# Kernel optimization log

Measured on AMD Instinct MI355X. Metric: run time of the kernel, lower is better.

The kernel has to match this reference:

```python
import jax, jax.numpy as jnp
from jax import lax
import numpy as np

I, H, B, S = 512, 1024, 64, 512


def setup_inputs() -> dict:
    key = jax.random.key(0)
    ks = jax.random.split(key, 10)
    xav = lambda k, shape: jax.random.uniform(k, shape, jnp.float32, -1.0, 1.0) * jnp.sqrt(6.0 / (shape[0] + shape[1]))
    return {
        "x": jax.random.normal(ks[0], (B, S, I), jnp.float32),
        "wii": xav(ks[1], (I, H)), "bii": jnp.zeros((H,), jnp.float32),
        "whi": xav(ks[2], (H, H)), "bhi": jnp.zeros((H,), jnp.float32),
        "wif": xav(ks[3], (I, H)), "bif": jnp.zeros((H,), jnp.float32),
        "whf": xav(ks[4], (H, H)), "bhf": jnp.zeros((H,), jnp.float32),
        "wig": xav(ks[5], (I, H)), "big": jnp.zeros((H,), jnp.float32),
        "whg": xav(ks[6], (H, H)), "bhg": jnp.zeros((H,), jnp.float32),
        "wio": xav(ks[7], (I, H)), "bio": jnp.zeros((H,), jnp.float32),
        "who": xav(ks[8], (H, H)), "bho": jnp.zeros((H,), jnp.float32),
    }


def reference(x, wii, bii, whi, bhi, wif, bif, whf, bhf,
              wig, big, whg, bhg, wio, bio, who, bho):
    b, s, _ = x.shape
    h = wii.shape[1]
    # Fuse the four per-gate GEMMs into single (I,4H) / (H,4H) GEMMs — same math.
    Wx = jnp.concatenate([wii, wif, wig, wio], axis=1)   # (I, 4H)
    Wh = jnp.concatenate([whi, whf, whg, who], axis=1)   # (H, 4H)
    bb = jnp.concatenate([bii + bhi, bif + bhf, big + bhg, bio + bho])  # (4H,)
    xs = jnp.swapaxes(x, 0, 1)                            # (S, B, I)
    x_proj = jnp.einsum('sbi,ik->sbk', xs, Wx) + bb       # (S, B, 4H)

    def step(carry, xp):
        h_t, c_t = carry
        gates = xp + h_t @ Wh                             # (B, 4H)
        i_t, f_t, g_t, o_t = jnp.split(gates, 4, axis=-1)
        i_t = jax.nn.sigmoid(i_t)
        f_t = jax.nn.sigmoid(f_t)
        g_t = jnp.tanh(g_t)
        o_t = jax.nn.sigmoid(o_t)
        c_t = f_t * c_t + i_t * g_t
        h_t = o_t * jnp.tanh(c_t)
        return (h_t, c_t), None

    h0 = jnp.zeros((b, h), x.dtype)
    c0 = jnp.zeros((b, h), x.dtype)
    (h_T, c_T), _ = lax.scan(step, (h0, c0), x_proj)
    return (h_T, c_T)
```

## Files before the change

kernel.cpp:

```cpp
#include <hip/hip_runtime.h>
#include <hip/hip_bf16.h>
#include <stdint.h>

typedef __bf16 bf16_t;
typedef bf16_t bf16x8 __attribute__((ext_vector_type(8)));
typedef float  f32x4  __attribute__((ext_vector_type(4)));
typedef float  f32x16 __attribute__((ext_vector_type(16)));

#define I_DIM 512
#define H_DIM 1024
#define B_DIM 64
#define S_DIM 512
#define G4    4096
#define CHUNK 16
#define NCHUNK (S_DIM / CHUNK)
#define XPSLOT_ELEMS ((size_t)CHUNK * 64 * G4)

#define O_WXT   0x0000000ULL
#define O_WHTF  0x0400000ULL
#define O_BIAS  0x0C00000ULL
#define O_HBUF  0x0D00000ULL
#define O_BAR   0x0D40000ULL
#define O_XP    0x1200000ULL

#define XPD_IDX(c)  (2048 + (c) * 64)
#define CONS_IDX(c) (4096 + (c) * 64)

__device__ __forceinline__ float sigm(float x)      { return 1.f / (1.f + __expf(-x)); }
__device__ __forceinline__ float tanh_fast(float x) { return 1.f - 2.f / (__expf(2.f * x) + 1.f); }


__global__ void k_pack_wx(const float* __restrict__ w0, const float* __restrict__ w1,
                          const float* __restrict__ w2, const float* __restrict__ w3,
                          bf16_t* __restrict__ wxt) {
    int tid = blockIdx.x * 256 + threadIdx.x;
    int k = tid >> 12;
    int p = tid & 4095;
    int q = p >> 5, g = (p >> 3) & 3, jj = p & 7;
    int j = q * 8 + jj;
    const float* src = (g == 0) ? w0 : (g == 1) ? w1 : (g == 2) ? w2 : w3;
    wxt[(size_t)p * I_DIM + k] = (bf16_t)src[k * H_DIM + j];
}

__global__ void k_pack_whf(const float* __restrict__ w0, const float* __restrict__ w1,
                           const float* __restrict__ w2, const float* __restrict__ w3,
                           bf16_t* __restrict__ whtf) {
    int idx = blockIdx.x * 256 + threadIdx.x;
    int e    = idx & 7;
    int lane = (idx >> 3) & 63;
    int ks   = (idx >> 9) & 63;
    int q    = idx >> 15;
    int k = ks * 16 + (lane >> 5) * 8 + e;
    int c = lane & 31;
    int g = c >> 3, jj = c & 7;
    int j = q * 8 + jj;
    const float* src = (g == 0) ? w0 : (g == 1) ? w1 : (g == 2) ? w2 : w3;
    whtf[idx] = (bf16_t)src[k * H_DIM + j];
}

__global__ void k_pack_bias(const float* bi0, const float* bh0, const float* bi1, const float* bh1,
                            const float* bi2, const float* bh2, const float* bi3, const float* bh3,
                            float* __restrict__ bias) {
    int p = blockIdx.x * 256 + threadIdx.x;
    int q = p >> 5, g = (p >> 3) & 3, jj = p & 7;
    int j = q * 8 + jj;
    const float* a = (g == 0) ? bi0 : (g == 1) ? bi1 : (g == 2) ? bi2 : bi3;
    const float* b = (g == 0) ? bh0 : (g == 1) ? bh1 : (g == 2) ? bh2 : bh3;
    bias[p] = a[j] + b[j];
}

__global__ __launch_bounds__(256, 2) void k_mega(
    const float* __restrict__ x, const bf16_t* __restrict__ wxt,
    const float* __restrict__ bias, const bf16_t* __restrict__ whtf,
    bf16_t* __restrict__ xp, bf16_t* __restrict__ hbuf,
    float* __restrict__ out, uint32_t* __restrict__ bar)
{
    __shared__ float Pl[4][16][64];
    __shared__ __align__(16) bf16_t Hlds[256];
    __shared__ __align__(16) bf16_t Al[8 * 64 * 8];
    __shared__ __align__(16) bf16_t Bl[8 * 64 * 8];
    const int tid  = threadIdx.x;

    if (blockIdx.x >= 256) {
        const int xbid = blockIdx.x - 256;
        const int n0 = (xbid & 31) * 128;
        const int rt = (xbid >> 5) * 128;
        const int wv = tid >> 6;
        const int lane = tid & 63;
        const int mq = wv >> 1, nq = wv & 1;
        const int l15 = lane & 15, quad = lane >> 4;

        for (int sc = 0; sc < NCHUNK; ++sc) {
            if (sc >= 2) {
                if (tid == 0) {
                    while (__hip_atomic_load(&bar[CONS_IDX(sc - 2)], __ATOMIC_RELAXED,
                                             __HIP_MEMORY_SCOPE_AGENT) < 256u)
                        __builtin_amdgcn_s_sleep(2);
                }
                __syncthreads();
            }
            bf16_t* xps = xp + (size_t)(sc & 1) * XPSLOT_ELEMS;
            const int r_base = sc * (CHUNK * 64);

            f32x4 acc[4][4] = {};
            for (int kk = 0; kk < I_DIM; kk += 32) {
                __syncthreads();
                #pragma unroll
                for (int sidx = 0; sidx < 2; ++sidx) {
                    int s = tid + sidx * 256;
                    int mt = s >> 6, l = s & 63;
                    int m = l & 15, kb = (l >> 4) * 8;
                    int r = r_base + rt + mt * 16 + m;
                    int b = r & 63, si = r >> 6;
                    const float* gp = x + ((size_t)(b * S_DIM + si)) * I_DIM + kk + kb;
                    float4 v0 = *(const float4*)gp;
                    float4 v1 = *(const float4*)(gp + 4);
                    bf16x8 a;
                    a[0] = (bf16_t)v0.x; a[1] = (bf16_t)v0.y; a[2] = (bf16_t)v0.z; a[3] = (bf16_t)v0.w;
                    a[4] = (bf16_t)v1.x; a[5] = (bf16_t)v1.y; a[6] = (bf16_t)v1.z; a[7] = (bf16_t)v1.w;
                    *(bf16x8*)&Al[s * 8] = a;
                    bf16x8 bv = *(const bf16x8*)(wxt + (size_t)(n0 + mt * 16 + m) * I_DIM + kk + kb);
                    *(bf16x8*)&Bl[s * 8] = bv;
                }
                __syncthreads();
                bf16x8 af[4], bfr[4];
                #pragma unroll
                for (int mt = 0; mt < 4; ++mt) af[mt]  = *(bf16x8*)&Al[((mq * 4 + mt) * 64 + lane) * 8];
                #pragma unroll
                for (int nt = 0; nt < 4; ++nt) bfr[nt] = *(bf16x8*)&Bl[((nq * 4 + nt) * 64 + lane) * 8];
                #pragma unroll
                for (int mt = 0; mt < 4; ++mt)
                    #pragma unroll
                    for (int nt = 0; nt < 4; ++nt)
                        acc[mt][nt] = __builtin_amdgcn_mfma_f32_16x16x32_bf16(af[mt], bfr[nt], acc[mt][nt], 0, 0, 0);
            }
            #pragma unroll
            for (int nt = 0; nt < 4; ++nt) {
                int colg = n0 + nq * 64 + nt * 16 + l15;
                float bv = bias[colg];
                #pragma unroll
                for (int mt = 0; mt < 4; ++mt)
                    #pragma unroll
                    for (int r = 0; r < 4; ++r) {
                        int row = rt + mq * 64 + mt * 16 + quad * 4 + r;
                        bf16_t hb = (bf16_t)(acc[mt][nt][r] + bv);
                        __hip_atomic_store((uint16_t*)(xps + (size_t)row * G4 + colg),
                                           __builtin_bit_cast(unsigned short, hb),
                                           __ATOMIC_RELAXED, __HIP_MEMORY_SCOPE_AGENT);
                    }
            }
            asm volatile("s_waitcnt vmcnt(0)" ::: "memory");
            __syncthreads();
            if (tid == 0)
                __hip_atomic_fetch_add(&bar[XPD_IDX(sc)], 1u,
                                       __ATOMIC_RELAXED, __HIP_MEMORY_SCOPE_AGENT);
        }
        return;
    }

    __builtin_amdgcn_s_setprio(1);

    const int w    = tid >> 6;
    const int lane = tid & 63;
    const int bid  = blockIdx.x;
    const int q    = bid & 127;
    const int bh   = bid >> 7;

    const int col  = lane & 31;
    const int ksel = lane >> 5;
    const int gt   = (lane >> 3) & 3;
    const int jj   = lane & 7;

    uint32_t* grp  = bar + ((bh * 8 + (q & 7)) << 6);
    uint32_t* root = bar + 1024 + (bh << 6);

    int rrow[4];
    #pragma unroll
    for (int e = 0; e < 4; ++e) rrow[e] = e + 8 * w + 4 * ksel;

    const bf16_t* bb = whtf + ((size_t)q << 15) + (w << 13) + (lane << 3);
    bf16x8 bfr[16];
    #pragma unroll
    for (int i = 0; i < 16; ++i) bfr[i] = *(const bf16x8*)(bb + i * 512);

    float cst[4] = {0.f, 0.f, 0.f, 0.f};

    const int abase = (bh << 15) + (w << 13) + (lane << 3);

    for (int c = 0; c < NCHUNK; ++c) {
        if (tid == 0) {
            while (__hip_atomic_load(&bar[XPD_IDX(c)], __ATOMIC_RELAXED,
                                     __HIP_MEMORY_SCOPE_AGENT) < 256u)
                __builtin_amdgcn_s_sleep(2);
        }
        __syncthreads();
        const uint16_t* xpc = (const uint16_t*)(xp + (size_t)(c & 1) * XPSLOT_ELEMS);

        for (int tl = 0; tl < CHUNK; ++tl) {
            const int t = c * CHUNK + tl;

            const uint64_t* hsrc = (const uint64_t*)(hbuf + ((t & 1) << 16) + abase);
            uint64_t hl0[16], hl1[16];
            #pragma unroll
            for (int i = 0; i < 16; ++i) {
                hl0[i] = __hip_atomic_load(hsrc + i * 128,     __ATOMIC_RELAXED, __HIP_MEMORY_SCOPE_AGENT);
                hl1[i] = __hip_atomic_load(hsrc + i * 128 + 1, __ATOMIC_RELAXED, __HIP_MEMORY_SCOPE_AGENT);
            }

            bf16_t xpr[4];
            #pragma unroll
            for (int e = 0; e < 4; ++e) {
                unsigned short v = __hip_atomic_load(
                    &xpc[(size_t)(tl * 64 + bh * 32 + rrow[e]) * G4 + q * 32 + col],
                    __ATOMIC_RELAXED, __HIP_MEMORY_SCOPE_AGENT);
                xpr[e] = __builtin_bit_cast(bf16_t, v);
            }

            struct U2 { uint64_t a, b; };
            f32x16 acc0 = {}, acc1 = {}, acc2 = {}, acc3 = {};
            #pragma unroll
            for (int i = 0; i < 16; i += 4) {
                U2 t0{hl0[i + 0], hl1[i + 0]};
                U2 t1{hl0[i + 1], hl1[i + 1]};
                U2 t2{hl0[i + 2], hl1[i + 2]};
                U2 t3{hl0[i + 3], hl1[i + 3]};
                acc0 = __builtin_amdgcn_mfma_f32_32x32x16_bf16(__builtin_bit_cast(bf16x8, t0), bfr[i + 0], acc0, 0, 0, 0);
                acc1 = __builtin_amdgcn_mfma_f32_32x32x16_bf16(__builtin_bit_cast(bf16x8, t1), bfr[i + 1], acc1, 0, 0, 0);
                acc2 = __builtin_amdgcn_mfma_f32_32x32x16_bf16(__builtin_bit_cast(bf16x8, t2), bfr[i + 2], acc2, 0, 0, 0);
                acc3 = __builtin_amdgcn_mfma_f32_32x32x16_bf16(__builtin_bit_cast(bf16x8, t3), bfr[i + 3], acc3, 0, 0, 0);
            }
            f32x16 accs = acc0 + acc1 + acc2 + acc3;

            #pragma unroll
            for (int e = 0; e < 16; ++e) Pl[w][e][lane] = accs[e];
            __syncthreads();

            #pragma unroll
            for (int e = 0; e < 4; ++e) {
                int eg = w * 4 + e;
                float pre = Pl[0][eg][lane] + Pl[1][eg][lane] + Pl[2][eg][lane] + Pl[3][eg][lane];
                pre += (float)xpr[e];
                float a = (gt == 2) ? tanh_fast(pre) : sigm(pre);

                float fv = __shfl_xor(a, 8, 64);
                float gv = __shfl_xor(a, 16, 64);
                float ov = __shfl_xor(a, 24, 64);
                if (gt == 0) {
                    float cn = fv * cst[e] + a * gv;
                    float hv = ov * tanh_fast(cn);
                    cst[e] = cn;
                    Hlds[rrow[e] * 8 + jj] = (bf16_t)hv;
                    if (t == S_DIM - 1) {
                        int rowg = bh * 32 + rrow[e];
                        int j = q * 8 + jj;
                        out[rowg * H_DIM + j] = hv;
                        out[65536 + rowg * H_DIM + j] = cn;
                    }
                }
            }
            __syncthreads();

            if (w == 0) {
                uint64_t v = *(const uint64_t*)&Hlds[lane * 4];
                uint64_t* hdst = (uint64_t*)hbuf + (((t + 1) & 1) << 14)
                               + (bh << 13) + (q << 6) + lane;
                __hip_atomic_store(hdst, v, __ATOMIC_RELAXED, __HIP_MEMORY_SCOPE_AGENT);
                if (t < S_DIM - 1) {
                    asm volatile("s_waitcnt vmcnt(0)" ::: "memory");
                    if (lane == 0) {
                        uint32_t old = __hip_atomic_fetch_add(grp, 1u,
                                                              __ATOMIC_RELAXED, __HIP_MEMORY_SCOPE_AGENT);
                        if ((old & 15u) == 15u)
                            __hip_atomic_fetch_add(root, 1u,
                                                   __ATOMIC_RELAXED, __HIP_MEMORY_SCOPE_AGENT);
                        uint32_t target = (uint32_t)(8 * (t + 1));
                        while (__hip_atomic_load(root, __ATOMIC_RELAXED,
                                                 __HIP_MEMORY_SCOPE_AGENT) < target) {}
                    }
                }
            }
            if (t < S_DIM - 1) __syncthreads();
        }

        if (tid == 0)
            __hip_atomic_fetch_add(&bar[CONS_IDX(c)], 1u,
                                   __ATOMIC_RELAXED, __HIP_MEMORY_SCOPE_AGENT);
    }
}

extern "C" void kernel_launch(void* const* d_in, const int* in_sizes, int n_in,
                              void* d_out, int out_size, void* d_ws, size_t ws_size,
                              hipStream_t stream) {
    const float* x   = (const float*)d_in[0];
    const float* wii = (const float*)d_in[1];
    const float* bii = (const float*)d_in[2];
    const float* whi = (const float*)d_in[3];
    const float* bhi = (const float*)d_in[4];
    const float* wif = (const float*)d_in[5];
    const float* bif = (const float*)d_in[6];
    const float* whf = (const float*)d_in[7];
    const float* bhf = (const float*)d_in[8];
    const float* wig = (const float*)d_in[9];
    const float* big = (const float*)d_in[10];
    const float* whg = (const float*)d_in[11];
    const float* bhg = (const float*)d_in[12];
    const float* wio = (const float*)d_in[13];
    const float* bio = (const float*)d_in[14];
    const float* who = (const float*)d_in[15];
    const float* bho = (const float*)d_in[16];

    char* ws = (char*)d_ws;
    bf16_t*   wxt  = (bf16_t*)(ws + O_WXT);
    bf16_t*   whtf = (bf16_t*)(ws + O_WHTF);
    float*    bias = (float*)(ws + O_BIAS);
    bf16_t*   hbuf = (bf16_t*)(ws + O_HBUF);
    uint32_t* bar  = (uint32_t*)(ws + O_BAR);
    bf16_t*   xp   = (bf16_t*)(ws + O_XP);

    hipMemsetAsync(hbuf, 0, 256 * 1024, stream);
    hipMemsetAsync(bar,  0, 32 * 1024, stream);

    k_pack_wx<<<8192, 256, 0, stream>>>(wii, wif, wig, wio, wxt);
    k_pack_whf<<<16384, 256, 0, stream>>>(whi, whf, whg, who, whtf);
    k_pack_bias<<<16, 256, 0, stream>>>(bii, bhi, bif, bhf, big, bhg, bio, bho, bias);

    float* out = (float*)d_out;
    void* args[] = { (void*)&x, (void*)&wxt, (void*)&bias, (void*)&whtf,
                     (void*)&xp, (void*)&hbuf, (void*)&out, (void*)&bar };
    hipError_t err = hipLaunchCooperativeKernel((const void*)k_mega, dim3(512), dim3(256),
                                                args, 0, stream);
    if (err != hipSuccess) {
        k_mega<<<512, 256, 0, stream>>>(x, wxt, bias, whtf, xp, hbuf, out, bar);
    }
}
```

Baseline: 3.194 ms.

## Halve cooperative grid, giving each recurrent block two hidden-column groups

```diff
diff --git a/kernel.cpp b/kernel.cpp
--- a/kernel.cpp
+++ b/kernel.cpp
@@ -69,22 +69,20 @@
     bias[p] = a[j] + b[j];
 }
 
-__global__ __launch_bounds__(256, 2) void k_mega(
+__global__ __launch_bounds__(256, 1) void k_mega(
     const float* __restrict__ x, const bf16_t* __restrict__ wxt,
     const float* __restrict__ bias, const bf16_t* __restrict__ whtf,
     bf16_t* __restrict__ xp, bf16_t* __restrict__ hbuf,
     float* __restrict__ out, uint32_t* __restrict__ bar)
 {
-    __shared__ float Pl[4][16][64];
-    __shared__ __align__(16) bf16_t Hlds[256];
+    __shared__ float Pl[4][2][16][64];
+    __shared__ __align__(16) bf16_t Hlds[2][256];
     __shared__ __align__(16) bf16_t Al[8 * 64 * 8];
     __shared__ __align__(16) bf16_t Bl[8 * 64 * 8];
     const int tid  = threadIdx.x;
 
-    if (blockIdx.x >= 256) {
-        const int xbid = blockIdx.x - 256;
-        const int n0 = (xbid & 31) * 128;
-        const int rt = (xbid >> 5) * 128;
+    if (blockIdx.x >= 128) {
+        const int xbid = blockIdx.x - 128;
         const int wv = tid >> 6;
         const int lane = tid & 63;
         const int mq = wv >> 1, nq = wv & 1;
@@ -94,7 +92,7 @@
             if (sc >= 2) {
                 if (tid == 0) {
                     while (__hip_atomic_load(&bar[CONS_IDX(sc - 2)], __ATOMIC_RELAXED,
-                                             __HIP_MEMORY_SCOPE_AGENT) < 256u)
+                                             __HIP_MEMORY_SCOPE_AGENT) < 128u)
                         __builtin_amdgcn_s_sleep(2);
                 }
                 __syncthreads();
@@ -102,52 +100,58 @@
             bf16_t* xps = xp + (size_t)(sc & 1) * XPSLOT_ELEMS;
             const int r_base = sc * (CHUNK * 64);
 
-            f32x4 acc[4][4] = {};
-            for (int kk = 0; kk < I_DIM; kk += 32) {
-                __syncthreads();
+            for (int tt = 0; tt < 2; ++tt) {
+                const int tile = xbid * 2 + tt;
+                const int n0 = (tile & 31) * 128;
+                const int rt = (tile >> 5) * 128;
+
+                f32x4 acc[4][4] = {};
+                for (int kk = 0; kk < I_DIM; kk += 32) {
+                    __syncthreads();
+                    #pragma unroll
+                    for (int sidx = 0; sidx < 2; ++sidx) {
+                        int s = tid + sidx * 256;
+                        int mt = s >> 6, l = s & 63;
+                        int m = l & 15, kb = (l >> 4) * 8;
+                        int r = r_base + rt + mt * 16 + m;
+                        int b = r & 63, si = r >> 6;
+                        const float* gp = x + ((size_t)(b * S_DIM + si)) * I_DIM + kk + kb;
+                        float4 v0 = *(const float4*)gp;
+                        float4 v1 = *(const float4*)(gp + 4);
+                        bf16x8 a;
+                        a[0] = (bf16_t)v0.x; a[1] = (bf16_t)v0.y; a[2] = (bf16_t)v0.z; a[3] = (bf16_t)v0.w;
+                        a[4] = (bf16_t)v1.x; a[5] = (bf16_t)v1.y; a[6] = (bf16_t)v1.z; a[7] = (bf16_t)v1.w;
+                        *(bf16x8*)&Al[s * 8] = a;
+                        bf16x8 bv = *(const bf16x8*)(wxt + (size_t)(n0 + mt * 16 + m) * I_DIM + kk + kb);
+                        *(bf16x8*)&Bl[s * 8] = bv;
+                    }
+                    __syncthreads();
+                    bf16x8 af[4], bfr[4];
+                    #pragma unroll
+                    for (int mt = 0; mt < 4; ++mt) af[mt]  = *(bf16x8*)&Al[((mq * 4 + mt) * 64 + lane) * 8];
+                    #pragma unroll
+                    for (int nt = 0; nt < 4; ++nt) bfr[nt] = *(bf16x8*)&Bl[((nq * 4 + nt) * 64 + lane) * 8];
+                    #pragma unroll
+                    for (int mt = 0; mt < 4; ++mt)
+                        #pragma unroll
+                        for (int nt = 0; nt < 4; ++nt)
+                            acc[mt][nt] = __builtin_amdgcn_mfma_f32_16x16x32_bf16(af[mt], bfr[nt], acc[mt][nt], 0, 0, 0);
+                }
                 #pragma unroll
-                for (int sidx = 0; sidx < 2; ++sidx) {
-                    int s = tid + sidx * 256;
-                    int mt = s >> 6, l = s & 63;
-                    int m = l & 15, kb = (l >> 4) * 8;
-                    int r = r_base + rt + mt * 16 + m;
-                    int b = r & 63, si = r >> 6;
-                    const float* gp = x + ((size_t)(b * S_DIM + si)) * I_DIM + kk + kb;
-                    float4 v0 = *(const float4*)gp;
-                    float4 v1 = *(const float4*)(gp + 4);
-                    bf16x8 a;
-                    a[0] = (bf16_t)v0.x; a[1] = (bf16_t)v0.y; a[2] = (bf16_t)v0.z; a[3] = (bf16_t)v0.w;
-                    a[4] = (bf16_t)v1.x; a[5] = (bf16_t)v1.y; a[6] = (bf16_t)v1.z; a[7] = (bf16_t)v1.w;
-                    *(bf16x8*)&Al[s * 8] = a;
-                    bf16x8 bv = *(const bf16x8*)(wxt + (size_t)(n0 + mt * 16 + m) * I_DIM + kk + kb);
-                    *(bf16x8*)&Bl[s * 8] = bv;
-                }
-                __syncthreads();
-                bf16x8 af[4], bfr[4];
-                #pragma unroll
-                for (int mt = 0; mt < 4; ++mt) af[mt]  = *(bf16x8*)&Al[((mq * 4 + mt) * 64 + lane) * 8];
-                #pragma unroll
-                for (int nt = 0; nt < 4; ++nt) bfr[nt] = *(bf16x8*)&Bl[((nq * 4 + nt) * 64 + lane) * 8];
-                #pragma unroll
-                for (int mt = 0; mt < 4; ++mt)
-                    #pragma unroll
-                    for (int nt = 0; nt < 4; ++nt)
-                        acc[mt][nt] = __builtin_amdgcn_mfma_f32_16x16x32_bf16(af[mt], bfr[nt], acc[mt][nt], 0, 0, 0);
-            }
-            #pragma unroll
-            for (int nt = 0; nt < 4; ++nt) {
-                int colg = n0 + nq * 64 + nt * 16 + l15;
-                float bv = bias[colg];
-                #pragma unroll
-                for (int mt = 0; mt < 4; ++mt)
-                    #pragma unroll
-                    for (int r = 0; r < 4; ++r) {
-                        int row = rt + mq * 64 + mt * 16 + quad * 4 + r;
-                        bf16_t hb = (bf16_t)(acc[mt][nt][r] + bv);
-                        __hip_atomic_store((uint16_t*)(xps + (size_t)row * G4 + colg),
-                                           __builtin_bit_cast(unsigned short, hb),
-                                           __ATOMIC_RELAXED, __HIP_MEMORY_SCOPE_AGENT);
-                    }
+                for (int nt = 0; nt < 4; ++nt) {
+                    int colg = n0 + nq * 64 + nt * 16 + l15;
+                    float bv = bias[colg];
+                    #pragma unroll
+                    for (int mt = 0; mt < 4; ++mt)
+                        #pragma unroll
+                        for (int r = 0; r < 4; ++r) {
+                            int row = rt + mq * 64 + mt * 16 + quad * 4 + r;
+                            bf16_t hb = (bf16_t)(acc[mt][nt][r] + bv);
+                            __hip_atomic_store((uint16_t*)(xps + (size_t)row * G4 + colg),
+                                               __builtin_bit_cast(unsigned short, hb),
+                                               __ATOMIC_RELAXED, __HIP_MEMORY_SCOPE_AGENT);
+                        }
+                }
             }
             asm volatile("s_waitcnt vmcnt(0)" ::: "memory");
             __syncthreads();
@@ -158,39 +162,42 @@
         return;
     }
 
-    __builtin_amdgcn_s_setprio(1);
-
     const int w    = tid >> 6;
     const int lane = tid & 63;
     const int bid  = blockIdx.x;
-    const int q    = bid & 127;
-    const int bh   = bid >> 7;
+    const int qp   = bid & 63;
+    const int q0   = qp * 2;
+    const int bh   = bid >> 6;
 
     const int col  = lane & 31;
     const int ksel = lane >> 5;
     const int gt   = (lane >> 3) & 3;
     const int jj   = lane & 7;
 
-    uint32_t* grp  = bar + ((bh * 8 + (q & 7)) << 6);
+    uint32_t* grp  = bar + ((bh * 8 + (qp & 7)) << 6);
     uint32_t* root = bar + 1024 + (bh << 6);
 
     int rrow[4];
     #pragma unroll
     for (int e = 0; e < 4; ++e) rrow[e] = e + 8 * w + 4 * ksel;
 
-    const bf16_t* bb = whtf + ((size_t)q << 15) + (w << 13) + (lane << 3);
-    bf16x8 bfr[16];
-    #pragma unroll
-    for (int i = 0; i < 16; ++i) bfr[i] = *(const bf16x8*)(bb + i * 512);
-
-    float cst[4] = {0.f, 0.f, 0.f, 0.f};
+    bf16x8 bfr0[16], bfr1[16];
+    {
+        const bf16_t* bb0 = whtf + ((size_t)q0 << 15) + (w << 13) + (lane << 3);
+        const bf16_t* bb1 = whtf + ((size_t)(q0 + 1) << 15) + (w << 13) + (lane << 3);
+        #pragma unroll
+        for (int i = 0; i < 16; ++i) { bfr0[i] = *(const bf16x8*)(bb0 + i * 512);
+                                       bfr1[i] = *(const bf16x8*)(bb1 + i * 512); }
+    }
+
+    float cst[2][4] = {};
 
     const int abase = (bh << 15) + (w << 13) + (lane << 3);
 
     for (int c = 0; c < NCHUNK; ++c) {
         if (tid == 0) {
             while (__hip_atomic_load(&bar[XPD_IDX(c)], __ATOMIC_RELAXED,
-                                     __HIP_MEMORY_SCOPE_AGENT) < 256u)
+                                     __HIP_MEMORY_SCOPE_AGENT) < 128u)
                 __builtin_amdgcn_s_sleep(2);
         }
         __syncthreads();
@@ -207,70 +214,79 @@
                 hl1[i] = __hip_atomic_load(hsrc + i * 128 + 1, __ATOMIC_RELAXED, __HIP_MEMORY_SCOPE_AGENT);
             }
 
-            bf16_t xpr[4];
-            #pragma unroll
-            for (int e = 0; e < 4; ++e) {
-                unsigned short v = __hip_atomic_load(
-                    &xpc[(size_t)(tl * 64 + bh * 32 + rrow[e]) * G4 + q * 32 + col],
-                    __ATOMIC_RELAXED, __HIP_MEMORY_SCOPE_AGENT);
-                xpr[e] = __builtin_bit_cast(bf16_t, v);
-            }
+            bf16_t xpr[2][4];
+            #pragma unroll
+            for (int qb = 0; qb < 2; ++qb)
+                #pragma unroll
+                for (int e = 0; e < 4; ++e) {
+                    unsigned short v = __hip_atomic_load(
+                        &xpc[(size_t)(tl * 64 + bh * 32 + rrow[e]) * G4 + (q0 + qb) * 32 + col],
+                        __ATOMIC_RELAXED, __HIP_MEMORY_SCOPE_AGENT);
+                    xpr[qb][e] = __builtin_bit_cast(bf16_t, v);
+                }
 
             struct U2 { uint64_t a, b; };
-            f32x16 acc0 = {}, acc1 = {}, acc2 = {}, acc3 = {};
-            #pragma unroll
-            for (int i = 0; i < 16; i += 4) {
-                U2 t0{hl0[i + 0], hl1[i + 0]};
+            f32x16 a00 = {}, a01 = {}, a10 = {}, a11 = {};
+            #pragma unroll
+            for (int i = 0; i < 16; i += 2) {
+                U2 t0{hl0[i],     hl1[i]};
                 U2 t1{hl0[i + 1], hl1[i + 1]};
-                U2 t2{hl0[i + 2], hl1[i + 2]};
-                U2 t3{hl0[i + 3], hl1[i + 3]};
-                acc0 = __builtin_amdgcn_mfma_f32_32x32x16_bf16(__builtin_bit_cast(bf16x8, t0), bfr[i + 0], acc0, 0, 0, 0);
-                acc1 = __builtin_amdgcn_mfma_f32_32x32x16_bf16(__builtin_bit_cast(bf16x8, t1), bfr[i + 1], acc1, 0, 0, 0);
-                acc2 = __builtin_amdgcn_mfma_f32_32x32x16_bf16(__builtin_bit_cast(bf16x8, t2), bfr[i + 2], acc2, 0, 0, 0);
-                acc3 = __builtin_amdgcn_mfma_f32_32x32x16_bf16(__builtin_bit_cast(bf16x8, t3), bfr[i + 3], acc3, 0, 0, 0);
-            }
-            f32x16 accs = acc0 + acc1 + acc2 + acc3;
-
-            #pragma unroll
-            for (int e = 0; e < 16; ++e) Pl[w][e][lane] = accs[e];
+                bf16x8 A0 = __builtin_bit_cast(bf16x8, t0);
+                bf16x8 A1 = __builtin_bit_cast(bf16x8, t1);
+                a00 = __builtin_amdgcn_mfma_f32_32x32x16_bf16(A0, bfr0[i],     a00, 0, 0, 0);
+                a10 = __builtin_amdgcn_mfma_f32_32x32x16_bf16(A0, bfr1[i],     a10, 0, 0, 0);
+                a01 = __builtin_amdgcn_mfma_f32_32x32x16_bf16(A1, bfr0[i + 1], a01, 0, 0, 0);
+                a11 = __builtin_amdgcn_mfma_f32_32x32x16_bf16(A1, bfr1[i + 1], a11, 0, 0, 0);
+            }
+            f32x16 acc_q0 = a00 + a01;
+            f32x16 acc_q1 = a10 + a11;
+
+            #pragma unroll
+            for (int e = 0; e < 16; ++e) { Pl[w][0][e][lane] = acc_q0[e];
+                                           Pl[w][1][e][lane] = acc_q1[e]; }
             __syncthreads();
 
             #pragma unroll
-            for (int e = 0; e < 4; ++e) {
-                int eg = w * 4 + e;
-                float pre = Pl[0][eg][lane] + Pl[1][eg][lane] + Pl[2][eg][lane] + Pl[3][eg][lane];
-                pre += (float)xpr[e];
-                float a = (gt == 2) ? tanh_fast(pre) : sigm(pre);
-
-                float fv = __shfl_xor(a, 8, 64);
-                float gv = __shfl_xor(a, 16, 64);
-                float ov = __shfl_xor(a, 24, 64);
-                if (gt == 0) {
-                    float cn = fv * cst[e] + a * gv;
-                    float hv = ov * tanh_fast(cn);
-                    cst[e] = cn;
-                    Hlds[rrow[e] * 8 + jj] = (bf16_t)hv;
-                    if (t == S_DIM - 1) {
-                        int rowg = bh * 32 + rrow[e];
-                        int j = q * 8 + jj;
-                        out[rowg * H_DIM + j] = hv;
-                        out[65536 + rowg * H_DIM + j] = cn;
+            for (int qb = 0; qb < 2; ++qb) {
+                #pragma unroll
+                for (int e = 0; e < 4; ++e) {
+                    int eg = w * 4 + e;
+                    float pre = Pl[0][qb][eg][lane] + Pl[1][qb][eg][lane]
+                              + Pl[2][qb][eg][lane] + Pl[3][qb][eg][lane];
+                    pre += (float)xpr[qb][e];
+                    float a = (gt == 2) ? tanh_fast(pre) : sigm(pre);
+
+                    float fv = __shfl_xor(a, 8, 64);
+                    float gv = __shfl_xor(a, 16, 64);
+                    float ov = __shfl_xor(a, 24, 64);
+                    if (gt == 0) {
+                        float cn = fv * cst[qb][e] + a * gv;
+                        float hv = ov * tanh_fast(cn);
+                        cst[qb][e] = cn;
+                        Hlds[qb][rrow[e] * 8 + jj] = (bf16_t)hv;
+                        if (t == S_DIM - 1) {
+                            int rowg = bh * 32 + rrow[e];
+                            int j = (q0 + qb) * 8 + jj;
+                            out[rowg * H_DIM + j] = hv;
+                            out[65536 + rowg * H_DIM + j] = cn;
+                        }
                     }
                 }
             }
             __syncthreads();
 
             if (w == 0) {
-                uint64_t v = *(const uint64_t*)&Hlds[lane * 4];
-                uint64_t* hdst = (uint64_t*)hbuf + (((t + 1) & 1) << 14)
-                               + (bh << 13) + (q << 6) + lane;
-                __hip_atomic_store(hdst, v, __ATOMIC_RELAXED, __HIP_MEMORY_SCOPE_AGENT);
+                uint64_t v0 = *(const uint64_t*)&Hlds[0][lane * 4];
+                uint64_t v1 = *(const uint64_t*)&Hlds[1][lane * 4];
+                uint64_t* hb = (uint64_t*)hbuf + (((t + 1) & 1) << 14) + (bh << 13);
+                __hip_atomic_store(hb + (q0 << 6) + lane,       v0, __ATOMIC_RELAXED, __HIP_MEMORY_SCOPE_AGENT);
+                __hip_atomic_store(hb + ((q0 + 1) << 6) + lane, v1, __ATOMIC_RELAXED, __HIP_MEMORY_SCOPE_AGENT);
                 if (t < S_DIM - 1) {
                     asm volatile("s_waitcnt vmcnt(0)" ::: "memory");
                     if (lane == 0) {
                         uint32_t old = __hip_atomic_fetch_add(grp, 1u,
                                                               __ATOMIC_RELAXED, __HIP_MEMORY_SCOPE_AGENT);
-                        if ((old & 15u) == 15u)
+                        if ((old & 7u) == 7u)
                             __hip_atomic_fetch_add(root, 1u,
                                                    __ATOMIC_RELAXED, __HIP_MEMORY_SCOPE_AGENT);
                         uint32_t target = (uint32_t)(8 * (t + 1));
@@ -327,9 +343,9 @@
     float* out = (float*)d_out;
     void* args[] = { (void*)&x, (void*)&wxt, (void*)&bias, (void*)&whtf,
                      (void*)&xp, (void*)&hbuf, (void*)&out, (void*)&bar };
-    hipError_t err = hipLaunchCooperativeKernel((const void*)k_mega, dim3(512), dim3(256),
+    hipError_t err = hipLaunchCooperativeKernel((const void*)k_mega, dim3(256), dim3(256),
                                                 args, 0, stream);
     if (err != hipSuccess) {
-        k_mega<<<512, 256, 0, stream>>>(x, wxt, bias, whtf, xp, hbuf, out, bar);
+        k_mega<<<256, 256, 0, stream>>>(x, wxt, bias, whtf, xp, hbuf, out, bar);
     }
 }
```

Result: slower. 3.786 ms (+18.5%).
